# Optimization experiments

Measured on AMD Instinct MI355X. Metric: run time of the kernel, lower is better.

## Reference

```python
import jax, jax.numpy as jnp
import numpy as np

N, D, B = 500000, 256, 2048

def setup_inputs() -> dict:
    key = jax.random.key(0)
    k1, k2, k3 = jax.random.split(key, 3)
    x = jax.random.normal(k1, (N, D), dtype=jnp.float32)
    batch_id = jnp.sort(jax.random.randint(k2, (N,), 0, B, dtype=jnp.int64))
    gate_w = jax.random.normal(k3, (D, 1), dtype=jnp.float32) * (1.0 / np.sqrt(D))
    gate_b = jnp.zeros((1,), dtype=jnp.float32)
    return {"x": x, "batch_id": batch_id, "batch_size": B, "gate_w": gate_w, "gate_b": gate_b}

def reference(x, batch_id, batch_size, gate_w, gate_b):
    # gate: Linear(D,1) + Sigmoid -> (N, 1)
    weights = jax.nn.sigmoid(x @ gate_w + gate_b)  # (N, 1)
    weighted = x * weights                          # (N, D)
    # scatter_add by graph id -> (B, D)
    pooled = jax.ops.segment_sum(weighted, batch_id, num_segments=batch_size)
    return pooled
```

## Files before the change

kernel.cpp:

```cpp
#include <hip/hip_runtime.h>

#define D_DIM   256
#define NBLOCKS 1024
#define NWAVES  (NBLOCKS * 4)

typedef float v4f __attribute__((ext_vector_type(4)));

__device__ __forceinline__ float dot4(v4f v, v4f w) {
    return v[0]*w[0] + v[1]*w[1] + v[2]*w[2] + v[3]*w[3];
}
__device__ __forceinline__ float sigmoidf_(float t) {
    return 1.0f / (1.0f + __expf(-t));
}
__device__ __forceinline__ v4f vzero() {
    v4f z = {0.f, 0.f, 0.f, 0.f};
    return z;
}
__device__ __forceinline__ void flush_acc(float* __restrict__ out, int b,
                                          int lane, v4f acc) {
    float* p = out + (size_t)b * D_DIM + lane * 4;
    unsafeAtomicAdd(p + 0, acc[0]);
    unsafeAtomicAdd(p + 1, acc[1]);
    unsafeAtomicAdd(p + 2, acc[2]);
    unsafeAtomicAdd(p + 3, acc[3]);
}

__device__ __forceinline__ void prefetch_group(v4f& c0, v4f& c1, v4f& c2, v4f& c3,
                                               int4& cb,
                                               const float* px, const int* pb,
                                               bool pred) {
    if (pred) {
        c0 = __builtin_nontemporal_load((const v4f*)(px + 0 * D_DIM));
        c1 = __builtin_nontemporal_load((const v4f*)(px + 1 * D_DIM));
        c2 = __builtin_nontemporal_load((const v4f*)(px + 2 * D_DIM));
        c3 = __builtin_nontemporal_load((const v4f*)(px + 3 * D_DIM));
        cb = *(const int4*)pb;
    }
}

__device__ __forceinline__ void process_group(v4f c0, v4f c1, v4f c2, v4f c3,
                                              int4 cb, v4f w4, float bias,
                                              v4f& acc, int& cur,
                                              float* __restrict__ out, int lane) {
    float s0 = dot4(c0, w4);
    float s1 = dot4(c1, w4);
    float s2 = dot4(c2, w4);
    float s3 = dot4(c3, w4);
    #pragma unroll
    for (int off = 32; off > 0; off >>= 1) {
        s0 += __shfl_xor(s0, off, 64);
        s1 += __shfl_xor(s1, off, 64);
        s2 += __shfl_xor(s2, off, 64);
        s3 += __shfl_xor(s3, off, 64);
    }
    float g0 = sigmoidf_(s0 + bias);
    float g1 = sigmoidf_(s1 + bias);
    float g2 = sigmoidf_(s2 + bias);
    float g3 = sigmoidf_(s3 + bias);

    if ((cb.x == cur) & (cb.y == cur) & (cb.z == cur) & (cb.w == cur)) {
        acc += c0 * g0 + c1 * g1 + c2 * g2 + c3 * g3;
    } else {
        if (cb.x != cur) { flush_acc(out, cur, lane, acc); acc = vzero(); cur = cb.x; }
        acc += c0 * g0;
        if (cb.y != cur) { flush_acc(out, cur, lane, acc); acc = vzero(); cur = cb.y; }
        acc += c1 * g1;
        if (cb.z != cur) { flush_acc(out, cur, lane, acc); acc = vzero(); cur = cb.z; }
        acc += c2 * g2;
        if (cb.w != cur) { flush_acc(out, cur, lane, acc); acc = vzero(); cur = cb.w; }
        acc += c3 * g3;
    }
}

__global__ __launch_bounds__(256) void attentive_readout_kernel(
    const float* __restrict__ x,
    const int* __restrict__ bid,
    const float* __restrict__ gw,
    const float* __restrict__ gb,
    float* __restrict__ out,
    int n)
{
    int gtid = blockIdx.x * blockDim.x + threadIdx.x;
    int wave = gtid >> 6;
    int lane = threadIdx.x & 63;

    const int total_groups = n >> 2;
    const int base = total_groups / NWAVES;
    const int rem  = total_groups % NWAVES;
    const int g0   = wave * base + (wave < rem ? wave : rem);
    const int ng   = base + (wave < rem ? 1 : 0);
    if (ng <= 0) return;

    const long long r0 = (long long)g0 << 2;

    const v4f w4 = *(const v4f*)(gw + lane * 4);
    const float bias = gb[0];

    v4f acc = vzero();
    int cur = bid[r0];

    const float* pxa = x + (size_t)r0 * D_DIM + lane * 4;
    const float* pxb = pxa + 4 * D_DIM;
    const int*   pba = bid + r0;
    const int*   pbb = pba + 4;

    v4f a0, a1, a2, a3, b0, b1, b2, b3;
    int4 ab, bb;
    prefetch_group(a0, a1, a2, a3, ab, pxa, pba, true);
    prefetch_group(b0, b1, b2, b3, bb, pxb, pbb, ng > 1);

    int g = 0;
    for (; g + 2 <= ng; g += 2) {
        process_group(a0, a1, a2, a3, ab, w4, bias, acc, cur, out, lane);
        prefetch_group(a0, a1, a2, a3, ab, pxa + 8 * D_DIM, pba + 8,
                       g + 2 < ng);
        pxa += 8 * D_DIM; pba += 8;

        process_group(b0, b1, b2, b3, bb, w4, bias, acc, cur, out, lane);
        prefetch_group(b0, b1, b2, b3, bb, pxb + 8 * D_DIM, pbb + 8,
                       g + 3 < ng);
        pxb += 8 * D_DIM; pbb += 8;
    }
    if (g < ng) {
        process_group(a0, a1, a2, a3, ab, w4, bias, acc, cur, out, lane);
    }

    flush_acc(out, cur, lane, acc);
}

extern "C" void kernel_launch(void* const* d_in, const int* in_sizes, int n_in,
                              void* d_out, int out_size, void* d_ws, size_t ws_size,
                              hipStream_t stream) {
    const float* x   = (const float*)d_in[0];
    const int*   bid = (const int*)d_in[1];
    const float* gw  = (const float*)d_in[3];
    const float* gb  = (const float*)d_in[4];
    float*       out = (float*)d_out;

    const int n = in_sizes[0] / D_DIM;

    hipMemsetAsync(d_out, 0, (size_t)out_size * sizeof(float), stream);

    attentive_readout_kernel<<<NBLOCKS, 256, 0, stream>>>(
        x, bid, gw, gb, out, n);
}
```

Baseline: 98.33 us.

## Merge gate reductions across four rows, add uniform-segment fast path, triple-buffer loads

Result: slower. 104.2 us (+6.0%).

```diff
diff --git a/kernel.cpp b/kernel.cpp
--- a/kernel.cpp
+++ b/kernel.cpp
@@ -25,50 +25,69 @@
     unsafeAtomicAdd(p + 3, acc[3]);
 }
 
-__device__ __forceinline__ void prefetch_group(v4f& c0, v4f& c1, v4f& c2, v4f& c3,
-                                               int4& cb,
-                                               const float* px, const int* pb,
-                                               bool pred) {
+template<int CTRL>
+__device__ __forceinline__ float qperm(float v) {
+    return __int_as_float(
+        __builtin_amdgcn_mov_dpp(__float_as_int(v), CTRL, 0xF, 0xF, 0));
+}
+
+__device__ __forceinline__ void gate4(float s0, float s1, float s2, float s3,
+                                      bool l1, bool l2, float bias,
+                                      float& g0, float& g1, float& g2, float& g3) {
+    s0 += __shfl_xor(s0, 1, 64); s0 += __shfl_xor(s0, 2, 64);
+    s1 += __shfl_xor(s1, 1, 64); s1 += __shfl_xor(s1, 2, 64);
+    s2 += __shfl_xor(s2, 1, 64); s2 += __shfl_xor(s2, 2, 64);
+    s3 += __shfl_xor(s3, 1, 64); s3 += __shfl_xor(s3, 2, 64);
+    float va = l1 ? s1 : s0;
+    float vb = l1 ? s3 : s2;
+    float v  = l2 ? vb : va;
+    v += __shfl_xor(v, 4, 64);
+    v += __shfl_xor(v, 8, 64);
+    v += __shfl_xor(v, 16, 64);
+    v += __shfl_xor(v, 32, 64);
+    float g = sigmoidf_(v + bias);
+    g0 = qperm<0x00>(g);
+    g1 = qperm<0x55>(g);
+    g2 = qperm<0xAA>(g);
+    g3 = qperm<0xFF>(g);
+}
+
+struct Grp { v4f c0, c1, c2, c3; };
+
+__device__ __forceinline__ void pf(Grp& G, const float* px, bool pred) {
     if (pred) {
-        c0 = __builtin_nontemporal_load((const v4f*)(px + 0 * D_DIM));
-        c1 = __builtin_nontemporal_load((const v4f*)(px + 1 * D_DIM));
-        c2 = __builtin_nontemporal_load((const v4f*)(px + 2 * D_DIM));
-        c3 = __builtin_nontemporal_load((const v4f*)(px + 3 * D_DIM));
-        cb = *(const int4*)pb;
+        G.c0 = __builtin_nontemporal_load((const v4f*)(px + 0 * D_DIM));
+        G.c1 = __builtin_nontemporal_load((const v4f*)(px + 1 * D_DIM));
+        G.c2 = __builtin_nontemporal_load((const v4f*)(px + 2 * D_DIM));
+        G.c3 = __builtin_nontemporal_load((const v4f*)(px + 3 * D_DIM));
     }
 }
 
-__device__ __forceinline__ void process_group(v4f c0, v4f c1, v4f c2, v4f c3,
-                                              int4 cb, v4f w4, float bias,
-                                              v4f& acc, int& cur,
-                                              float* __restrict__ out, int lane) {
-    float s0 = dot4(c0, w4);
-    float s1 = dot4(c1, w4);
-    float s2 = dot4(c2, w4);
-    float s3 = dot4(c3, w4);
-    #pragma unroll
-    for (int off = 32; off > 0; off >>= 1) {
-        s0 += __shfl_xor(s0, off, 64);
-        s1 += __shfl_xor(s1, off, 64);
-        s2 += __shfl_xor(s2, off, 64);
-        s3 += __shfl_xor(s3, off, 64);
-    }
-    float g0 = sigmoidf_(s0 + bias);
-    float g1 = sigmoidf_(s1 + bias);
-    float g2 = sigmoidf_(s2 + bias);
-    float g3 = sigmoidf_(s3 + bias);
+__device__ __forceinline__ void proc_u(const Grp& G, v4f w4, float bias,
+                                       bool l1, bool l2, v4f& acc) {
+    float g0, g1, g2, g3;
+    gate4(dot4(G.c0, w4), dot4(G.c1, w4), dot4(G.c2, w4), dot4(G.c3, w4),
+          l1, l2, bias, g0, g1, g2, g3);
+    acc += G.c0 * g0 + G.c1 * g1 + G.c2 * g2 + G.c3 * g3;
+}
 
+__device__ __forceinline__ void proc_g(const Grp& G, int4 cb, v4f w4, float bias,
+                                       bool l1, bool l2, v4f& acc, int& cur,
+                                       float* __restrict__ out, int lane) {
+    float g0, g1, g2, g3;
+    gate4(dot4(G.c0, w4), dot4(G.c1, w4), dot4(G.c2, w4), dot4(G.c3, w4),
+          l1, l2, bias, g0, g1, g2, g3);
     if ((cb.x == cur) & (cb.y == cur) & (cb.z == cur) & (cb.w == cur)) {
-        acc += c0 * g0 + c1 * g1 + c2 * g2 + c3 * g3;
+        acc += G.c0 * g0 + G.c1 * g1 + G.c2 * g2 + G.c3 * g3;
     } else {
         if (cb.x != cur) { flush_acc(out, cur, lane, acc); acc = vzero(); cur = cb.x; }
-        acc += c0 * g0;
+        acc += G.c0 * g0;
         if (cb.y != cur) { flush_acc(out, cur, lane, acc); acc = vzero(); cur = cb.y; }
-        acc += c1 * g1;
+        acc += G.c1 * g1;
         if (cb.z != cur) { flush_acc(out, cur, lane, acc); acc = vzero(); cur = cb.z; }
-        acc += c2 * g2;
+        acc += G.c2 * g2;
         if (cb.w != cur) { flush_acc(out, cur, lane, acc); acc = vzero(); cur = cb.w; }
-        acc += c3 * g3;
+        acc += G.c3 * g3;
     }
 }
 
@@ -87,45 +106,75 @@
     const int total_groups = n >> 2;
     const int base = total_groups / NWAVES;
     const int rem  = total_groups % NWAVES;
-    const int g0   = wave * base + (wave < rem ? wave : rem);
+    const int G0   = wave * base + (wave < rem ? wave : rem);
     const int ng   = base + (wave < rem ? 1 : 0);
     if (ng <= 0) return;
 
-    const long long r0 = (long long)g0 << 2;
+    const long long r0   = (long long)G0 << 2;
+    const long long rend = r0 + ((long long)ng << 2);
 
     const v4f w4 = *(const v4f*)(gw + lane * 4);
     const float bias = gb[0];
+    const bool l1 = lane & 1;
+    const bool l2 = lane & 2;
 
     v4f acc = vzero();
-    int cur = bid[r0];
+    const int bfirst = bid[r0];
+    const int blast  = bid[rend - 1];
 
-    const float* pxa = x + (size_t)r0 * D_DIM + lane * 4;
-    const float* pxb = pxa + 4 * D_DIM;
-    const int*   pba = bid + r0;
-    const int*   pbb = pba + 4;
+    const float* base_px = x + (size_t)r0 * D_DIM + lane * 4;
 
-    v4f a0, a1, a2, a3, b0, b1, b2, b3;
-    int4 ab, bb;
-    prefetch_group(a0, a1, a2, a3, ab, pxa, pba, true);
-    prefetch_group(b0, b1, b2, b3, bb, pxb, pbb, ng > 1);
+    Grp A, B, C;
+    const float* pA = base_px;
+    const float* pB = base_px + 4 * D_DIM;
+    const float* pC = base_px + 8 * D_DIM;
 
-    int g = 0;
-    for (; g + 2 <= ng; g += 2) {
-        process_group(a0, a1, a2, a3, ab, w4, bias, acc, cur, out, lane);
-        prefetch_group(a0, a1, a2, a3, ab, pxa + 8 * D_DIM, pba + 8,
-                       g + 2 < ng);
-        pxa += 8 * D_DIM; pba += 8;
+    if (bfirst == blast) {
+        pf(A, pA, true);
+        pf(B, pB, ng > 1);
+        pf(C, pC, ng > 2);
+        int g = 0;
+        for (; g + 3 <= ng; g += 3) {
+            proc_u(A, w4, bias, l1, l2, acc);
+            pf(A, pA + 12 * D_DIM, g + 3 < ng); pA += 12 * D_DIM;
+            proc_u(B, w4, bias, l1, l2, acc);
+            pf(B, pB + 12 * D_DIM, g + 4 < ng); pB += 12 * D_DIM;
+            proc_u(C, w4, bias, l1, l2, acc);
+            pf(C, pC + 12 * D_DIM, g + 5 < ng); pC += 12 * D_DIM;
+        }
+        if (g < ng)     proc_u(A, w4, bias, l1, l2, acc);
+        if (g + 1 < ng) proc_u(B, w4, bias, l1, l2, acc);
+        flush_acc(out, bfirst, lane, acc);
+    } else {
+        int cur = bfirst;
+        const int* qA = bid + r0;
+        const int* qB = qA + 4;
+        const int* qC = qA + 8;
+        int4 ab, bb, cb;
+        pf(A, pA, true);            ab = *(const int4*)qA;
+        pf(B, pB, ng > 1); if (ng > 1) bb = *(const int4*)qB;
+        pf(C, pC, ng > 2); if (ng > 2) cb = *(const int4*)qC;
+        int g = 0;
+        for (; g + 3 <= ng; g += 3) {
+            proc_g(A, ab, w4, bias, l1, l2, acc, cur, out, lane);
+            pf(A, pA + 12 * D_DIM, g + 3 < ng);
+            if (g + 3 < ng) ab = *(const int4*)(qA + 12);
+            pA += 12 * D_DIM; qA += 12;
 
-        process_group(b0, b1, b2, b3, bb, w4, bias, acc, cur, out, lane);
-        prefetch_group(b0, b1, b2, b3, bb, pxb + 8 * D_DIM, pbb + 8,
-                       g + 3 < ng);
-        pxb += 8 * D_DIM; pbb += 8;
+            proc_g(B, bb, w4, bias, l1, l2, acc, cur, out, lane);
+            pf(B, pB + 12 * D_DIM, g + 4 < ng);
+            if (g + 4 < ng) bb = *(const int4*)(qB + 12);
+            pB += 12 * D_DIM; qB += 12;
+
+            proc_g(C, cb, w4, bias, l1, l2, acc, cur, out, lane);
+            pf(C, pC + 12 * D_DIM, g + 5 < ng);
+            if (g + 5 < ng) cb = *(const int4*)(qC + 12);
+            pC += 12 * D_DIM; qC += 12;
+        }
+        if (g < ng)     proc_g(A, ab, w4, bias, l1, l2, acc, cur, out, lane);
+        if (g + 1 < ng) proc_g(B, bb, w4, bias, l1, l2, acc, cur, out, lane);
+        flush_acc(out, cur, lane, acc);
     }
-    if (g < ng) {
-        process_group(a0, a1, a2, a3, ab, w4, bias, acc, cur, out, lane);
-    }
-
-    flush_acc(out, cur, lane, acc);
 }
 
 extern "C" void kernel_launch(void* const* d_in, const int* in_sizes, int n_in,
```
